# Kernel tuning notes

Measured on AMD Instinct MI355X. Metric: run time of the kernel, lower is better.

Reference implementation:

```python
import jax, jax.numpy as jnp
import numpy as np

N_NODES = 100000
N_REL = 8
N_EDGES = 80000
IN_F, HID, OUT = 128, 32, 2
N_GRAPHS = 64


def setup_inputs() -> dict:
    key = jax.random.key(0)
    ks = jax.random.split(key, 12)
    x = jax.random.normal(ks[0], (N_NODES, IN_F), dtype=jnp.float32)
    src = jax.random.randint(ks[1], (N_REL, N_EDGES), 0, N_NODES, dtype=jnp.int32)
    dst = jax.random.randint(ks[2], (N_REL, N_EDGES), 0, N_NODES, dtype=jnp.int32)
    graph_ids = jax.random.randint(ks[3], (N_NODES,), 0, N_GRAPHS, dtype=jnp.int32)
    W1 = jax.random.normal(ks[4], (N_REL, IN_F, HID), dtype=jnp.float32) / np.sqrt(IN_F)
    b1 = jnp.zeros((N_REL, HID), dtype=jnp.float32)
    W2 = jax.random.normal(ks[5], (N_REL, HID, HID), dtype=jnp.float32) / np.sqrt(HID)
    b2 = jnp.zeros((N_REL, HID), dtype=jnp.float32)
    Wc = jax.random.normal(ks[6], (HID, OUT), dtype=jnp.float32) / np.sqrt(HID)
    bc = jnp.zeros((OUT,), dtype=jnp.float32)
    return {"x": x, "src": src, "dst": dst, "graph_ids": graph_ids,
            "num_graphs": N_GRAPHS, "W1": W1, "b1": b1, "W2": W2, "b2": b2,
            "Wc": Wc, "bc": bc}


def _hetero_conv(h, src, dst, W, b, n_nodes):
    """HeteroGraphConv(sum) of per-relation GraphConv(norm='both')."""
    n_rel = W.shape[0]
    out = jnp.zeros((n_nodes, W.shape[2]), dtype=h.dtype)
    ones_e = jnp.ones((src.shape[1],), dtype=h.dtype)
    for r in range(n_rel):  # small fixed relation set
        s, d = src[r], dst[r]
        # symmetric normalization with degree clamped to >= 1 (DGL behavior)
        deg_out = jnp.maximum(jax.ops.segment_sum(ones_e, s, num_segments=n_nodes), 1.0)
        deg_in = jnp.maximum(jax.ops.segment_sum(ones_e, d, num_segments=n_nodes), 1.0)
        hn = h * jax.lax.rsqrt(deg_out)[:, None]      # [N, F_in]
        hw = hn @ W[r]                                # project first (F_in >= F_out)
        agg = jax.ops.segment_sum(hw[s], d, num_segments=n_nodes)  # scatter-sum to dst
        out = out + agg * jax.lax.rsqrt(deg_in)[:, None] + b[r]
    return out


def reference(x, src, dst, graph_ids, num_graphs, W1, b1, W2, b2, Wc, bc):
    n = x.shape[0]
    h = jax.nn.relu(_hetero_conv(x, src, dst, W1, b1, n))
    h = _hetero_conv(h, src, dst, W2, b2, n)
    # per-graph mean pooling over nodes
    sums = jax.ops.segment_sum(h, graph_ids, num_segments=num_graphs)
    cnts = jnp.maximum(jax.ops.segment_sum(jnp.ones((n,), h.dtype), graph_ids,
                                           num_segments=num_graphs), 1.0)
    pooled = sums / cnts[:, None]
    return pooled @ Wc + bc
```

## Files before the change

kernel.cpp:

```cpp
#include <hip/hip_runtime.h>


#define N_NODES 100000
#define N_REL   8
#define N_EDGES 80000
#define IN_F    128
#define HID     32
#define N_GRAPHS 64
#define NCAT    (N_REL * HID)
#define N_KEYS  (N_NODES * N_REL)
#define TOT_E   (N_REL * N_EDGES)
#define DEG_BLOCKS  (TOT_E / 256)
#define GEMM_BLOCKS ((N_NODES / 16 + 3) / 4)

constexpr int TILE = 256;
constexpr int KC   = 32;

typedef __attribute__((ext_vector_type(8))) short bf16x8;
typedef __attribute__((ext_vector_type(4))) float f32x4;

__device__ __forceinline__ ushort f2bf(float v) {
  unsigned u = __builtin_bit_cast(unsigned, v);
  u = (u + 0x7fffu + ((u >> 16) & 1u)) >> 16;
  return (ushort)u;
}
__device__ __forceinline__ float bf2f(ushort h) {
  unsigned u = ((unsigned)h) << 16;
  return __builtin_bit_cast(float, u);
}

__global__ __launch_bounds__(256) void rsqrt_kernel(float* __restrict__ p, int count) {
  int i = blockIdx.x * 256 + threadIdx.x;
  if (i < count) {
    int d = ((const int*)p)[i];
    p[i] = rsqrtf((float)(d < 1 ? 1 : d));
  }
}

__global__ __launch_bounds__(256) void prep_w_kernel(const float* __restrict__ W1, const float* __restrict__ W2,
                                                     const float* __restrict__ Wc,
                                                     ushort* __restrict__ Wt1, ushort* __restrict__ Vt) {
  int i = blockIdx.x * 256 + threadIdx.x;
  if (i < NCAT * IN_F) {
    int n = i >> 7, k = i & 127;
    int r = n >> 5, j = n & 31;
    Wt1[i] = f2bf(W1[r * (IN_F * HID) + k * HID + j]);
  } else {
    int q = i - NCAT * IN_F;
    if (q < 16 * HID) {
      int n = q >> 5, k = q & 31;
      int r = n >> 1, c = n & 1;
      float s = 0.f;
#pragma unroll
      for (int j = 0; j < HID; j++) s += W2[r * (HID * HID) + k * HID + j] * Wc[j * 2 + c];
      Vt[q] = f2bf(s);
    }
  }
}

__global__ __launch_bounds__(256, 4) void fused_deg_gemm1(const int* __restrict__ src, const int* __restrict__ dst,
                                                          int* __restrict__ dego, int* __restrict__ cnt,
                                                          int* __restrict__ epos,
                                                          const float* __restrict__ A, const ushort* __restrict__ Bt,
                                                          ushort* __restrict__ Y, int M) {
  __shared__ ushort smem[17408];
  int bid = blockIdx.x;
  int isg, rid;
  if (bid < 2 * GEMM_BLOCKS) { isg = !(bid & 1); rid = bid >> 1; }
  else { isg = 0; rid = GEMM_BLOCKS + (bid - 2 * GEMM_BLOCKS); }

  if (!isg) {
    int i = rid * 256 + (int)threadIdx.x;
    int s = src[i], d = dst[i];
    int r = i / N_EDGES;
    atomicAdd(&dego[r * N_NODES + s], 1);
    epos[i] = atomicAdd(&cnt[d * N_REL + r], 1);
    return;
  }

  int wave = __builtin_amdgcn_readfirstlane(threadIdx.x >> 6);
  int lane = threadIdx.x & 63;
  int t = threadIdx.x;
  int m0 = (rid * 4 + wave) * 16;
  int me = (m0 <= M - 16) ? m0 : (M - 16);
  int row = lane & 15, quad = lane >> 4;

  bf16x8 af[4];
#pragma unroll
  for (int kq = 0; kq < 4; kq++) {
    const float* ap = &A[(size_t)(me + row) * IN_F + kq * 32 + quad * 8];
    float4 a0 = *(const float4*)ap;
    float4 a1 = *(const float4*)(ap + 4);
    bf16x8 a;
    a[0] = (short)f2bf(a0.x); a[1] = (short)f2bf(a0.y); a[2] = (short)f2bf(a0.z); a[3] = (short)f2bf(a0.w);
    a[4] = (short)f2bf(a1.x); a[5] = (short)f2bf(a1.y); a[6] = (short)f2bf(a1.z); a[7] = (short)f2bf(a1.w);
    af[kq] = a;
  }

  f32x4 acc[16];
#pragma unroll
  for (int nt = 0; nt < 16; nt++) acc[nt] = (f32x4){0.f, 0.f, 0.f, 0.f};

  for (int p = 0; p < 2; p++) {
    __syncthreads();
    const ushort* bsrc = Bt + (size_t)p * (128 * IN_F);
#pragma unroll
    for (int i = 0; i < 8; i++) {
      int c = t + i * 256;
      int rr2 = c >> 4, cc = c & 15;
      uint4 v = *(const uint4*)&bsrc[rr2 * IN_F + cc * 8];
      *(uint4*)&smem[rr2 * 136 + cc * 8] = v;
    }
    __syncthreads();
#pragma unroll
    for (int kq = 0; kq < 4; kq++) {
#pragma unroll
      for (int nt2 = 0; nt2 < 8; nt2++) {
        bf16x8 b = *(const bf16x8*)&smem[(nt2 * 16 + row) * 136 + kq * 32 + quad * 8];
        acc[p * 8 + nt2] = __builtin_amdgcn_mfma_f32_16x16x32_bf16(af[kq], b, acc[p * 8 + nt2], 0, 0, 0);
      }
    }
  }
  __syncthreads();

  ushort* myt = &smem[wave * 4160];
#pragma unroll
  for (int nt = 0; nt < 16; nt++) {
#pragma unroll
    for (int i = 0; i < 4; i++)
      myt[(quad * 4 + i) * 260 + nt * 16 + row] = f2bf(acc[nt][i]);
  }
  if (m0 <= M - 16) {
    ushort* ybase = &Y[(size_t)m0 * NCAT];
#pragma unroll
    for (int k = 0; k < 8; k++) {
      int g = k * 512 + lane * 8;
      int r2 = g >> 8, c2 = g & 255;
      const ushort* sp = &myt[r2 * 260 + c2];
      uint4 v;
      v.x = *(const uint*)(sp + 0);
      v.y = *(const uint*)(sp + 2);
      v.z = *(const uint*)(sp + 4);
      v.w = *(const uint*)(sp + 6);
      *(uint4*)&ybase[g] = v;
    }
  }
}

__global__ __launch_bounds__(256) void scan1_kernel(const int* __restrict__ in, int* __restrict__ out,
                                                    int* __restrict__ partial, int n) {
  __shared__ int ts[256];
  int b0 = blockIdx.x * 1024;
  int t = threadIdx.x;
  int v[4]; int s = 0;
#pragma unroll
  for (int k = 0; k < 4; k++) {
    int idx = b0 + t * 4 + k;
    v[k] = s;
    s += (idx < n) ? in[idx] : 0;
  }
  ts[t] = s;
  __syncthreads();
  for (int off = 1; off < 256; off <<= 1) {
    int xv = (t >= off) ? ts[t - off] : 0;
    __syncthreads();
    ts[t] += xv;
    __syncthreads();
  }
  int texcl = (t == 0) ? 0 : ts[t - 1];
#pragma unroll
  for (int k = 0; k < 4; k++) {
    int idx = b0 + t * 4 + k;
    if (idx < n) out[idx] = texcl + v[k];
  }
  if (t == 255) partial[blockIdx.x] = ts[255];
}

__global__ __launch_bounds__(256) void scan2_kernel(int* __restrict__ partial, int nb) {
  __shared__ int ts[256];
  int t = threadIdx.x;
  int v[4]; int s = 0;
#pragma unroll
  for (int k = 0; k < 4; k++) {
    int idx = t * 4 + k;
    v[k] = s;
    s += (idx < nb) ? partial[idx] : 0;
  }
  ts[t] = s;
  __syncthreads();
  for (int off = 1; off < 256; off <<= 1) {
    int xv = (t >= off) ? ts[t - off] : 0;
    __syncthreads();
    ts[t] += xv;
    __syncthreads();
  }
  int texcl = (t == 0) ? 0 : ts[t - 1];
#pragma unroll
  for (int k = 0; k < 4; k++) {
    int idx = t * 4 + k;
    if (idx < nb) partial[idx] = texcl + v[k];
  }
}

__global__ __launch_bounds__(256) void scan3_kernel(int* __restrict__ out, const int* __restrict__ partial, int n) {
  int i = blockIdx.x * 256 + threadIdx.x;
  if (i < n) out[i] += partial[i >> 10];
  if (i == 0) out[n] = TOT_E;
}

__global__ __launch_bounds__(256) void fill_kernel(const int* __restrict__ src, const int* __restrict__ dst,
                                                   const int* __restrict__ rp, const int* __restrict__ epos,
                                                   const float* __restrict__ rs_o,
                                                   int4* __restrict__ edata) {
  int i = blockIdx.x * 256 + threadIdx.x;
  int d = dst[i];
  int s = src[i];
  int r = i / N_EDGES;
  int key = d * N_REL + r;
  int b = rp[key];
  int c = rp[key + 1] - b;
  int t = b + epos[i];
  float w = rs_o[r * N_NODES + s] * rsqrtf((float)(c < 1 ? 1 : c));
  int4 e;
  e.x = s * NCAT + r * HID;
  e.y = s * 16 + r * 2;
  e.z = __builtin_bit_cast(int, w);
  e.w = 0;
  edata[t] = e;
}

__global__ __launch_bounds__(256) void gemm2_mfma(const ushort* __restrict__ H, const ushort* __restrict__ Vt,
                                                  float* __restrict__ Ys2, int M) {
  int wave = __builtin_amdgcn_readfirstlane(threadIdx.x >> 6);
  int lane = threadIdx.x & 63;
  int m0 = (blockIdx.x * 4 + wave) * 16;
  if (m0 >= M) return;
  int row = lane & 15, quad = lane >> 4;
  f32x4 acc = (f32x4){0.f, 0.f, 0.f, 0.f};
  bf16x8 a = *(const bf16x8*)&H[(size_t)(m0 + row) * HID + quad * 8];
  bf16x8 b = *(const bf16x8*)&Vt[row * HID + quad * 8];
  acc = __builtin_amdgcn_mfma_f32_16x16x32_bf16(a, b, acc, 0, 0, 0);
#pragma unroll
  for (int i = 0; i < 4; i++) {
    int m = m0 + quad * 4 + i;
    Ys2[(size_t)m * 16 + row] = acc[i];
  }
}

__global__ __launch_bounds__(256) void gather1_kernel(const ushort* __restrict__ Ys, const int4* __restrict__ edata,
                                                      const int* __restrict__ rp,
                                                      const float* __restrict__ b1, ushort* __restrict__ H) {
  int wave = __builtin_amdgcn_readfirstlane(threadIdx.x >> 6);
  int lane = threadIdx.x & 63;
  int d = blockIdx.x * 4 + wave;
  if (d >= N_NODES) return;
  int j = lane & 31, half = lane >> 5;
  int base = rp[d * N_REL], endp = rp[d * N_REL + N_REL];
  float sum = 0.f;
  for (int t = base + half; t < endp; t += 2) {
    int4 e = edata[t];
    float w = __builtin_bit_cast(float, e.z);
    sum += w * bf2f(Ys[(size_t)e.x + j]);
  }
  sum += __shfl_down(sum, 32);
  if (half == 0) {
    float sb = 0.f;
#pragma unroll
    for (int q = 0; q < N_REL; q++) sb += b1[q * HID + j];
    H[(size_t)d * HID + j] = f2bf(fmaxf(sum + sb, 0.f));
  }
}

__global__ __launch_bounds__(256) void gather2_pool_kernel(const float* __restrict__ Ys2,
                                                           const int4* __restrict__ edata,
                                                           const int* __restrict__ rp,
                                                           const int* __restrict__ gid,
                                                           float* __restrict__ gpool, float* __restrict__ gcnt) {
  __shared__ float lp[N_GRAPHS * 2];
  __shared__ float lc[N_GRAPHS];
  int t = threadIdx.x;
  if (t < N_GRAPHS * 2) lp[t] = 0.f;
  if (t < N_GRAPHS) lc[t] = 0.f;
  __syncthreads();
  for (int n = blockIdx.x * 256 + t; n < N_NODES; n += gridDim.x * 256) {
    int base = rp[n * N_REL], endp = rp[n * N_REL + N_REL];
    float z0 = 0.f, z1 = 0.f;
    for (int s = base; s < endp; s++) {
      int4 e = edata[s];
      float w = __builtin_bit_cast(float, e.z);
      float2 y = *(const float2*)&Ys2[e.y];
      z0 += w * y.x;
      z1 += w * y.y;
    }
    int g = gid[n];
    atomicAdd(&lp[g * 2 + 0], z0);
    atomicAdd(&lp[g * 2 + 1], z1);
    atomicAdd(&lc[g], 1.f);
  }
  __syncthreads();
  if (t < N_GRAPHS * 2) atomicAdd(&gpool[t], lp[t]);
  if (t < N_GRAPHS) atomicAdd(&gcnt[t], lc[t]);
}

__global__ void final_kernel(const float* __restrict__ gpool, const float* __restrict__ gcnt,
                             const float* __restrict__ b2, const float* __restrict__ Wc,
                             const float* __restrict__ bc, float* __restrict__ out) {
  int g = threadIdx.x;
  if (g >= N_GRAPHS) return;
  float c0 = 0.f, c1 = 0.f;
#pragma unroll
  for (int k = 0; k < HID; k++) {
    float sb = 0.f;
#pragma unroll
    for (int r = 0; r < N_REL; r++) sb += b2[r * HID + k];
    c0 += sb * Wc[k * 2 + 0];
    c1 += sb * Wc[k * 2 + 1];
  }
  float cntv = gcnt[g];
  if (cntv > 0.f) {
    out[g * 2 + 0] = gpool[g * 2 + 0] / cntv + c0 + bc[0];
    out[g * 2 + 1] = gpool[g * 2 + 1] / cntv + c1 + bc[1];
  } else {
    out[g * 2 + 0] = bc[0];
    out[g * 2 + 1] = bc[1];
  }
}

__global__ __launch_bounds__(256) void deg_kernel(const int* __restrict__ src, const int* __restrict__ dst,
                                                  int* __restrict__ dego, int* __restrict__ degi, int n_rel) {
  int i = blockIdx.x * 256 + threadIdx.x;
  if (i < n_rel * N_EDGES) {
    int r = i / N_EDGES;
    atomicAdd(&dego[r * N_NODES + src[i]], 1);
    atomicAdd(&degi[r * N_NODES + dst[i]], 1);
  }
}

__global__ __launch_bounds__(256) void proj1_kernel(const float* __restrict__ x, const float* __restrict__ W1r0,
                                                    const float* __restrict__ rs_o, float* __restrict__ hw,
                                                    int n0, int n1, int hw_nodes) {
  int rr = blockIdx.y;
  int nb = n0 + blockIdx.x * TILE;
  int t = threadIdx.x;
  __shared__ float xs[TILE][KC + 4];
  const float* __restrict__ Wr = W1r0 + (size_t)rr * (IN_F * HID);
  float acc[HID];
#pragma unroll
  for (int j = 0; j < HID; j++) acc[j] = 0.f;
  for (int kc = 0; kc < IN_F; kc += KC) {
    __syncthreads();
#pragma unroll
    for (int i = 0; i < (TILE * KC / 4) / 256; i++) {
      int q = t + i * 256;
      int nn = q >> 3, k4 = q & 7;
      int n = nb + nn;
      float4 v = make_float4(0.f, 0.f, 0.f, 0.f);
      if (n < n1) v = *(const float4*)&x[(size_t)n * IN_F + kc + k4 * 4];
      *(float4*)&xs[nn][k4 * 4] = v;
    }
    __syncthreads();
#pragma unroll
    for (int k4 = 0; k4 < KC / 4; k4++) {
      float4 xv = *(const float4*)&xs[t][k4 * 4];
      const float* wk = &Wr[(kc + k4 * 4) * HID];
#pragma unroll
      for (int j = 0; j < HID; j++) acc[j] += xv.x * wk[j];
#pragma unroll
      for (int j = 0; j < HID; j++) acc[j] += xv.y * wk[HID + j];
#pragma unroll
      for (int j = 0; j < HID; j++) acc[j] += xv.z * wk[2 * HID + j];
#pragma unroll
      for (int j = 0; j < HID; j++) acc[j] += xv.w * wk[3 * HID + j];
    }
  }
  int n = nb + t;
  if (n < n1) {
    float s = rs_o[(size_t)rr * N_NODES + n];
    float* o = &hw[((size_t)rr * hw_nodes + (n - n0)) * HID];
#pragma unroll
    for (int j4 = 0; j4 < HID / 4; j4++) {
      float4 v = make_float4(acc[j4 * 4] * s, acc[j4 * 4 + 1] * s, acc[j4 * 4 + 2] * s, acc[j4 * 4 + 3] * s);
      *(float4*)&o[j4 * 4] = v;
    }
  }
}

__global__ __launch_bounds__(256) void proj2_kernel(const float* __restrict__ acc1, const float* __restrict__ b1,
                                                    const float* __restrict__ W2r0, const float* __restrict__ rs_o,
                                                    float* __restrict__ hw, int n0, int n1, int hw_nodes) {
  int n = n0 + blockIdx.x * 256 + threadIdx.x;
  if (n >= n1) return;
  int rr = blockIdx.y;
  float h1[HID];
#pragma unroll
  for (int j4 = 0; j4 < HID / 4; j4++) {
    float4 v = *(const float4*)&acc1[(size_t)n * HID + j4 * 4];
    h1[j4 * 4 + 0] = v.x; h1[j4 * 4 + 1] = v.y; h1[j4 * 4 + 2] = v.z; h1[j4 * 4 + 3] = v.w;
  }
#pragma unroll
  for (int j = 0; j < HID; j++) {
    float sb = 0.f;
#pragma unroll
    for (int q = 0; q < N_REL; q++) sb += b1[q * HID + j];
    h1[j] = fmaxf(h1[j] + sb, 0.f);
  }
  const float* __restrict__ Wr = W2r0 + (size_t)rr * (HID * HID);
  float acc[HID];
#pragma unroll
  for (int j = 0; j < HID; j++) acc[j] = 0.f;
#pragma unroll
  for (int k = 0; k < HID; k++) {
    float hv = h1[k];
#pragma unroll
    for (int j = 0; j < HID; j++) acc[j] += hv * Wr[k * HID + j];
  }
  float s = rs_o[(size_t)rr * N_NODES + n];
  float* o = &hw[((size_t)rr * hw_nodes + (n - n0)) * HID];
#pragma unroll
  for (int j4 = 0; j4 < HID / 4; j4++) {
    float4 v = make_float4(acc[j4 * 4] * s, acc[j4 * 4 + 1] * s, acc[j4 * 4 + 2] * s, acc[j4 * 4 + 3] * s);
    *(float4*)&o[j4 * 4] = v;
  }
}

__global__ __launch_bounds__(256) void scatter_kernel(const float* __restrict__ hw, const int* __restrict__ src,
                                                      const int* __restrict__ dst, const float* __restrict__ rs_i,
                                                      float* __restrict__ acc, int nr, int n0, int n1, int hw_nodes) {
  long i = (long)blockIdx.x * 256 + threadIdx.x;
  long total = (long)nr * N_EDGES * HID;
  if (i >= total) return;
  int j = (int)(i & (HID - 1));
  long e = i >> 5;
  int rr = (int)(e / N_EDGES);
  int ee = (int)(e - (long)rr * N_EDGES);
  int s = src[rr * N_EDGES + ee];
  if (s < n0 || s >= n1) return;
  int d = dst[rr * N_EDGES + ee];
  float v = hw[((size_t)rr * hw_nodes + (s - n0)) * HID + j] * rs_i[(size_t)rr * N_NODES + d];
  atomicAdd(&acc[(size_t)d * HID + j], v);
}

__global__ __launch_bounds__(256) void pool_kernel(const float* __restrict__ acc2, const float* __restrict__ b2,
                                                   const int* __restrict__ gid, float* __restrict__ gpool,
                                                   float* __restrict__ gcnt) {
  __shared__ float lp[N_GRAPHS * HID];
  __shared__ float lc[N_GRAPHS];
  int t = threadIdx.x;
  for (int i = t; i < N_GRAPHS * HID; i += 256) lp[i] = 0.f;
  if (t < N_GRAPHS) lc[t] = 0.f;
  __syncthreads();
  int j = t & (HID - 1);
  int grp = t >> 5;
  float sb = 0.f;
#pragma unroll
  for (int q = 0; q < N_REL; q++) sb += b2[q * HID + j];
  for (int n = blockIdx.x * 8 + grp; n < N_NODES; n += gridDim.x * 8) {
    int g = gid[n];
    float v = acc2[(size_t)n * HID + j] + sb;
    atomicAdd(&lp[g * HID + j], v);
    if (j == 0) atomicAdd(&lc[g], 1.f);
  }
  __syncthreads();
  for (int i = t; i < N_GRAPHS * HID; i += 256) atomicAdd(&gpool[i], lp[i]);
  if (t < N_GRAPHS) atomicAdd(&gcnt[t], lc[t]);
}

__global__ void final3_kernel(const float* __restrict__ gpool, const float* __restrict__ gcnt,
                              const float* __restrict__ Wc, const float* __restrict__ bc,
                              float* __restrict__ out) {
  int g = threadIdx.x;
  if (g >= N_GRAPHS) return;
  float inv = 1.f / fmaxf(gcnt[g], 1.f);
  float o0 = bc[0], o1 = bc[1];
#pragma unroll
  for (int k = 0; k < HID; k++) {
    float p = gpool[g * HID + k] * inv;
    o0 += p * Wc[k * 2 + 0];
    o1 += p * Wc[k * 2 + 1];
  }
  out[g * 2 + 0] = o0;
  out[g * 2 + 1] = o1;
}

extern "C" void kernel_launch(void* const* d_in, const int* in_sizes, int n_in,
                              void* d_out, int out_size, void* d_ws, size_t ws_size,
                              hipStream_t stream) {
  const float* x  = (const float*)d_in[0];
  const int* src  = (const int*)d_in[1];
  const int* dst  = (const int*)d_in[2];
  const int* gid  = (const int*)d_in[3];
  const float* W1 = (const float*)d_in[5];
  const float* b1 = (const float*)d_in[6];
  const float* W2 = (const float*)d_in[7];
  const float* b2 = (const float*)d_in[8];
  const float* Wc = (const float*)d_in[9];
  const float* bc = (const float*)d_in[10];
  float* out = (float*)d_out;

  float* ws = (float*)d_ws;
  const size_t NF = (size_t)N_NODES * HID;
  const size_t RN = (size_t)N_REL * N_NODES;
  const size_t POOLF = N_GRAPHS * HID + N_GRAPHS;
  size_t wsf = ws_size / 4;

  const size_t T1_NEED = 22500000;

  if (wsf >= T1_NEED) {
    float* gpool = ws;
    float* gcnt  = gpool + N_GRAPHS * 2;
    float* rs_o  = gcnt + N_GRAPHS;
    int*   cnt   = (int*)(rs_o + RN);
    int*   epos  = cnt + N_KEYS;
    int*   rp    = epos + TOT_E;
    int*   part  = rp + N_KEYS + 8;
    int4*  edata = (int4*)(part + 1024);
    float* Ys2   = (float*)(edata + TOT_E);
    ushort* Ys   = (ushort*)(Ys2 + (size_t)N_NODES * 16);
    ushort* Hbf  = Ys + (size_t)N_NODES * NCAT;
    ushort* Wt1  = Hbf + (size_t)N_NODES * HID;
    ushort* Vt   = Wt1 + NCAT * IN_F;

    size_t zbytes = (N_GRAPHS * 3 + RN + (size_t)N_KEYS) * 4;
    hipMemsetAsync(ws, 0, zbytes, stream);

    prep_w_kernel<<<(NCAT * IN_F + 16 * HID + 255) / 256, 256, 0, stream>>>(W1, W2, Wc, Wt1, Vt);
    fused_deg_gemm1<<<DEG_BLOCKS + GEMM_BLOCKS, 256, 0, stream>>>(src, dst, (int*)rs_o, cnt, epos,
                                                                  x, Wt1, Ys, N_NODES);
    rsqrt_kernel<<<(int)((RN + 255) / 256), 256, 0, stream>>>(rs_o, (int)RN);

    int sblocks = (N_KEYS + 1023) / 1024;
    scan1_kernel<<<sblocks, 256, 0, stream>>>(cnt, rp, part, N_KEYS);
    scan2_kernel<<<1, 256, 0, stream>>>(part, sblocks);
    scan3_kernel<<<(N_KEYS + 255) / 256, 256, 0, stream>>>(rp, part, N_KEYS);
    fill_kernel<<<TOT_E / 256, 256, 0, stream>>>(src, dst, rp, epos, rs_o, edata);

    int gblocks = GEMM_BLOCKS;
    int nblocks = (N_NODES + 3) / 4;
    gather1_kernel<<<nblocks, 256, 0, stream>>>(Ys, edata, rp, b1, Hbf);
    gemm2_mfma<<<gblocks, 256, 0, stream>>>(Hbf, Vt, Ys2, N_NODES);
    gather2_pool_kernel<<<416, 256, 0, stream>>>(Ys2, edata, rp, gid, gpool, gcnt);
    final_kernel<<<1, 64, 0, stream>>>(gpool, gcnt, b2, Wc, bc, out);
  } else {
    float* acc1  = ws;
    float* acc2  = acc1 + NF;
    float* gpool = acc2 + NF;
    float* gcnt  = gpool + N_GRAPHS * HID;
    float* rsb   = ws + (2 * NF + POOLF);
    size_t zf = 2 * NF + POOLF;
    float* rs_o = rsb;
    float* rs_i = rsb + N_NODES;
    float* hw = rsb + 2 * N_NODES;
    size_t fixed3 = zf + 2 * N_NODES;
    size_t avail = (wsf > fixed3) ? (wsf - fixed3) : 0;
    long chunk = (long)(avail / HID) & ~255L;
    if (chunk < 256) chunk = 256;
    if (chunk > N_NODES) chunk = N_NODES;

    size_t zb = zf * 4; if (zb > ws_size) zb = ws_size;
    hipMemsetAsync(d_ws, 0, zb, stream);

    for (int layer = 0; layer < 2; layer++) {
      for (int r = 0; r < N_REL; r++) {
        hipMemsetAsync(rs_o, 0, 2 * N_NODES * 4, stream);
        deg_kernel<<<(N_EDGES + 255) / 256, 256, 0, stream>>>(src + (size_t)r * N_EDGES, dst + (size_t)r * N_EDGES,
                                                              (int*)rs_o, (int*)rs_i, 1);
        rsqrt_kernel<<<(2 * N_NODES + 255) / 256, 256, 0, stream>>>(rs_o, 2 * N_NODES);
        for (long n0 = 0; n0 < N_NODES; n0 += chunk) {
          long n1 = n0 + chunk; if (n1 > N_NODES) n1 = N_NODES;
          int tiles = (int)((n1 - n0 + TILE - 1) / TILE);
          if (layer == 0)
            proj1_kernel<<<dim3(tiles, 1), 256, 0, stream>>>(x, W1 + (size_t)r * IN_F * HID, rs_o, hw,
                                                             (int)n0, (int)n1, (int)chunk);
          else
            proj2_kernel<<<dim3(tiles, 1), 256, 0, stream>>>(acc1, b1, W2 + (size_t)r * HID * HID, rs_o, hw,
                                                             (int)n0, (int)n1, (int)chunk);
          long tot = (long)N_EDGES * HID;
          scatter_kernel<<<(int)((tot + 255) / 256), 256, 0, stream>>>(hw, src + (size_t)r * N_EDGES,
                                                                       dst + (size_t)r * N_EDGES, rs_i,
                                                                       layer == 0 ? acc1 : acc2,
                                                                       1, (int)n0, (int)n1, (int)chunk);
        }
      }
    }
    pool_kernel<<<256, 256, 0, stream>>>(acc2, b2, gid, gpool, gcnt);
    final3_kernel<<<1, 64, 0, stream>>>(gpool, gcnt, Wc, bc, out);
  }
}
```

Before: 260.5 us.

## Fuse second-layer projection into gather1 and drop scan3 and rsqrt kernels

Removes three kernel launches. The rsqrt pass is folded into fill_kernel by computing rsqrt of the out-degree from the raw count. The scan3 add-back pass is dropped: consumers now add the per-block partial sum on the fly. gemm2 is fused into gather1 with a shuffle-based 32x16 dot product per node, and the edge record shrinks from int4 to int2, with the Ys2 index derived from e.x. This saves launch overhead and the H round trip through memory, at the cost of extra partial lookups in every consumer and scalar FMA work in place of MFMA.

```diff
diff --git a/kernel.cpp b/kernel.cpp
--- a/kernel.cpp
+++ b/kernel.cpp
@@ -173,7 +173,10 @@
     int idx = b0 + t * 4 + k;
     if (idx < n) out[idx] = texcl + v[k];
   }
-  if (t == 255) partial[blockIdx.x] = ts[255];
+  if (t == 255) {
+    partial[blockIdx.x] = ts[255];
+    if (b0 + 1024 >= n) out[n] = ts[255];
+  }
 }
 
 __global__ __launch_bounds__(256) void scan2_kernel(int* __restrict__ partial, int nb) {
@@ -202,78 +205,71 @@
   }
 }
 
-__global__ __launch_bounds__(256) void scan3_kernel(int* __restrict__ out, const int* __restrict__ partial, int n) {
-  int i = blockIdx.x * 256 + threadIdx.x;
-  if (i < n) out[i] += partial[i >> 10];
-  if (i == 0) out[n] = TOT_E;
-}
-
 __global__ __launch_bounds__(256) void fill_kernel(const int* __restrict__ src, const int* __restrict__ dst,
-                                                   const int* __restrict__ rp, const int* __restrict__ epos,
-                                                   const float* __restrict__ rs_o,
-                                                   int4* __restrict__ edata) {
+                                                   const int* __restrict__ rp, const int* __restrict__ part,
+                                                   const int* __restrict__ epos, const int* __restrict__ dego,
+                                                   int2* __restrict__ edata) {
   int i = blockIdx.x * 256 + threadIdx.x;
   int d = dst[i];
   int s = src[i];
   int r = i / N_EDGES;
   int key = d * N_REL + r;
-  int b = rp[key];
-  int c = rp[key + 1] - b;
+  int b = rp[key] + part[key >> 10];
+  int k1 = key + 1;
+  int e2 = rp[k1] + part[k1 >> 10];
+  int c = e2 - b;
   int t = b + epos[i];
-  float w = rs_o[r * N_NODES + s] * rsqrtf((float)(c < 1 ? 1 : c));
-  int4 e;
+  int dg = dego[r * N_NODES + s];
+  float w = rsqrtf((float)(dg < 1 ? 1 : dg)) * rsqrtf((float)(c < 1 ? 1 : c));
+  int2 e;
   e.x = s * NCAT + r * HID;
-  e.y = s * 16 + r * 2;
-  e.z = __builtin_bit_cast(int, w);
-  e.w = 0;
+  e.y = __builtin_bit_cast(int, w);
   edata[t] = e;
 }
 
-__global__ __launch_bounds__(256) void gemm2_mfma(const ushort* __restrict__ H, const ushort* __restrict__ Vt,
-                                                  float* __restrict__ Ys2, int M) {
-  int wave = __builtin_amdgcn_readfirstlane(threadIdx.x >> 6);
-  int lane = threadIdx.x & 63;
-  int m0 = (blockIdx.x * 4 + wave) * 16;
-  if (m0 >= M) return;
-  int row = lane & 15, quad = lane >> 4;
-  f32x4 acc = (f32x4){0.f, 0.f, 0.f, 0.f};
-  bf16x8 a = *(const bf16x8*)&H[(size_t)(m0 + row) * HID + quad * 8];
-  bf16x8 b = *(const bf16x8*)&Vt[row * HID + quad * 8];
-  acc = __builtin_amdgcn_mfma_f32_16x16x32_bf16(a, b, acc, 0, 0, 0);
-#pragma unroll
-  for (int i = 0; i < 4; i++) {
-    int m = m0 + quad * 4 + i;
-    Ys2[(size_t)m * 16 + row] = acc[i];
-  }
-}
-
-__global__ __launch_bounds__(256) void gather1_kernel(const ushort* __restrict__ Ys, const int4* __restrict__ edata,
-                                                      const int* __restrict__ rp,
-                                                      const float* __restrict__ b1, ushort* __restrict__ H) {
+__global__ __launch_bounds__(256) void gather1_kernel(const ushort* __restrict__ Ys, const int2* __restrict__ edata,
+                                                      const int* __restrict__ rp, const int* __restrict__ part,
+                                                      const float* __restrict__ b1, const ushort* __restrict__ Vt,
+                                                      float* __restrict__ Ys2) {
   int wave = __builtin_amdgcn_readfirstlane(threadIdx.x >> 6);
   int lane = threadIdx.x & 63;
   int d = blockIdx.x * 4 + wave;
   if (d >= N_NODES) return;
   int j = lane & 31, half = lane >> 5;
-  int base = rp[d * N_REL], endp = rp[d * N_REL + N_REL];
+  int k0 = d * N_REL, k1 = k0 + N_REL;
+  int base = rp[k0] + part[k0 >> 10];
+  int endp = rp[k1] + part[k1 >> 10];
   float sum = 0.f;
   for (int t = base + half; t < endp; t += 2) {
-    int4 e = edata[t];
-    float w = __builtin_bit_cast(float, e.z);
+    int2 e = edata[t];
+    float w = __builtin_bit_cast(float, e.y);
     sum += w * bf2f(Ys[(size_t)e.x + j]);
   }
   sum += __shfl_down(sum, 32);
-  if (half == 0) {
-    float sb = 0.f;
-#pragma unroll
-    for (int q = 0; q < N_REL; q++) sb += b1[q * HID + j];
-    H[(size_t)d * HID + j] = f2bf(fmaxf(sum + sb, 0.f));
-  }
+  float sb = 0.f;
+#pragma unroll
+  for (int q = 0; q < N_REL; q++) sb += b1[q * HID + j];
+  float h = fmaxf(sum + sb, 0.f);
+  bf16x8 vrow[4];
+  if (lane < 16) {
+#pragma unroll
+    for (int q = 0; q < 4; q++) vrow[q] = *(const bf16x8*)&Vt[lane * HID + q * 8];
+  } else {
+#pragma unroll
+    for (int q = 0; q < 4; q++) vrow[q] = (bf16x8){0,0,0,0,0,0,0,0};
+  }
+  float acc = 0.f;
+#pragma unroll
+  for (int jj = 0; jj < 32; jj++) {
+    float hv = __shfl(h, jj);
+    acc += hv * bf2f((ushort)vrow[jj >> 3][jj & 7]);
+  }
+  if (lane < 16) Ys2[(size_t)d * 16 + lane] = acc;
 }
 
 __global__ __launch_bounds__(256) void gather2_pool_kernel(const float* __restrict__ Ys2,
-                                                           const int4* __restrict__ edata,
-                                                           const int* __restrict__ rp,
+                                                           const int2* __restrict__ edata,
+                                                           const int* __restrict__ rp, const int* __restrict__ part,
                                                            const int* __restrict__ gid,
                                                            float* __restrict__ gpool, float* __restrict__ gcnt) {
   __shared__ float lp[N_GRAPHS * 2];
@@ -283,12 +279,14 @@
   if (t < N_GRAPHS) lc[t] = 0.f;
   __syncthreads();
   for (int n = blockIdx.x * 256 + t; n < N_NODES; n += gridDim.x * 256) {
-    int base = rp[n * N_REL], endp = rp[n * N_REL + N_REL];
+    int k0 = n * N_REL, k1 = k0 + N_REL;
+    int base = rp[k0] + part[k0 >> 10];
+    int endp = rp[k1] + part[k1 >> 10];
     float z0 = 0.f, z1 = 0.f;
     for (int s = base; s < endp; s++) {
-      int4 e = edata[s];
-      float w = __builtin_bit_cast(float, e.z);
-      float2 y = *(const float2*)&Ys2[e.y];
+      int2 e = edata[s];
+      float w = __builtin_bit_cast(float, e.y);
+      float2 y = *(const float2*)&Ys2[e.x >> 4];
       z0 += w * y.x;
       z1 += w * y.y;
     }
@@ -508,37 +506,32 @@
   if (wsf >= T1_NEED) {
     float* gpool = ws;
     float* gcnt  = gpool + N_GRAPHS * 2;
-    float* rs_o  = gcnt + N_GRAPHS;
-    int*   cnt   = (int*)(rs_o + RN);
+    int*   dego  = (int*)(gcnt + N_GRAPHS);
+    int*   cnt   = dego + RN;
     int*   epos  = cnt + N_KEYS;
     int*   rp    = epos + TOT_E;
     int*   part  = rp + N_KEYS + 8;
-    int4*  edata = (int4*)(part + 1024);
+    int2*  edata = (int2*)(part + 1024);
     float* Ys2   = (float*)(edata + TOT_E);
     ushort* Ys   = (ushort*)(Ys2 + (size_t)N_NODES * 16);
-    ushort* Hbf  = Ys + (size_t)N_NODES * NCAT;
-    ushort* Wt1  = Hbf + (size_t)N_NODES * HID;
+    ushort* Wt1  = Ys + (size_t)N_NODES * NCAT;
     ushort* Vt   = Wt1 + NCAT * IN_F;
 
     size_t zbytes = (N_GRAPHS * 3 + RN + (size_t)N_KEYS) * 4;
     hipMemsetAsync(ws, 0, zbytes, stream);
 
     prep_w_kernel<<<(NCAT * IN_F + 16 * HID + 255) / 256, 256, 0, stream>>>(W1, W2, Wc, Wt1, Vt);
-    fused_deg_gemm1<<<DEG_BLOCKS + GEMM_BLOCKS, 256, 0, stream>>>(src, dst, (int*)rs_o, cnt, epos,
+    fused_deg_gemm1<<<DEG_BLOCKS + GEMM_BLOCKS, 256, 0, stream>>>(src, dst, dego, cnt, epos,
                                                                   x, Wt1, Ys, N_NODES);
-    rsqrt_kernel<<<(int)((RN + 255) / 256), 256, 0, stream>>>(rs_o, (int)RN);
 
     int sblocks = (N_KEYS + 1023) / 1024;
     scan1_kernel<<<sblocks, 256, 0, stream>>>(cnt, rp, part, N_KEYS);
     scan2_kernel<<<1, 256, 0, stream>>>(part, sblocks);
-    scan3_kernel<<<(N_KEYS + 255) / 256, 256, 0, stream>>>(rp, part, N_KEYS);
-    fill_kernel<<<TOT_E / 256, 256, 0, stream>>>(src, dst, rp, epos, rs_o, edata);
-
-    int gblocks = GEMM_BLOCKS;
+    fill_kernel<<<TOT_E / 256, 256, 0, stream>>>(src, dst, rp, part, epos, dego, edata);
+
     int nblocks = (N_NODES + 3) / 4;
-    gather1_kernel<<<nblocks, 256, 0, stream>>>(Ys, edata, rp, b1, Hbf);
-    gemm2_mfma<<<gblocks, 256, 0, stream>>>(Hbf, Vt, Ys2, N_NODES);
-    gather2_pool_kernel<<<416, 256, 0, stream>>>(Ys2, edata, rp, gid, gpool, gcnt);
+    gather1_kernel<<<nblocks, 256, 0, stream>>>(Ys, edata, rp, part, b1, Vt, Ys2);
+    gather2_pool_kernel<<<416, 256, 0, stream>>>(Ys2, edata, rp, part, gid, gpool, gcnt);
     final_kernel<<<1, 64, 0, stream>>>(gpool, gcnt, b2, Wc, bc, out);
   } else {
     float* acc1  = ws;
```

Result: no change. 259.2 us (-0.5%).
